# Kernel optimization log

Hardware: AMD Instinct MI355X
Metric: run time of the kernel (lower is better)

## Reference

```python
import jax, jax.numpy as jnp
import numpy as np

N, E, F_IN, F_E, H = 50000, 800000, 128, 16, 64
NEG_SLOPE = 0.2


def _glorot(key, shape):
    fan_in, fan_out = shape[0], shape[-1]
    lim = np.sqrt(6.0 / (fan_in + fan_out))
    return jax.random.uniform(key, shape, jnp.float32, -lim, lim)


def setup_inputs() -> dict:
    key = jax.random.key(0)
    ks = jax.random.split(key, 24)
    inp = {
        "x": jax.random.normal(ks[0], (N, F_IN), jnp.float32),
        "edge_index": jax.random.randint(ks[1], (2, E), 0, N, jnp.int64),
        "edge_attr": jax.random.normal(ks[2], (E, F_E), jnp.float32),
    }
    k = 3
    for i, f_in in zip((1, 2, 3), (F_IN, H, H)):
        inp[f"W{i}"] = _glorot(ks[k], (f_in, H)); k += 1
        inp[f"as{i}"] = _glorot(ks[k], (H,)); k += 1
        inp[f"ad{i}"] = _glorot(ks[k], (H,)); k += 1
        inp[f"We{i}"] = _glorot(ks[k], (F_E, H)); k += 1
        inp[f"ae{i}"] = _glorot(ks[k], (H,)); k += 1
        inp[f"b{i}"] = jnp.zeros((H,), jnp.float32)
        k += 1
    return inp


def gat_conv(x, src, dst, ea, W, a_s, a_d, We, a_e, b):
    # x: [N, f_in]; src/dst: [E'] (self-loops already appended); ea: [E', F_E]
    n = x.shape[0]
    h = x @ W                                   # [N, H]
    alpha_src = h @ a_s                          # [N]
    alpha_dst = h @ a_d                          # [N]
    alpha_e = (ea @ We) @ a_e                    # [E']
    alpha = alpha_src[src] + alpha_dst[dst] + alpha_e
    alpha = jnp.where(alpha > 0, alpha, NEG_SLOPE * alpha)  # leaky_relu
    # segment softmax over incoming edges of each dst node
    amax = jax.ops.segment_max(alpha, dst, num_segments=n)
    ex = jnp.exp(alpha - amax[dst])
    denom = jax.ops.segment_sum(ex, dst, num_segments=n)
    coef = ex / (denom[dst] + 1e-16)             # [E']
    out = jax.ops.segment_sum(h[src] * coef[:, None], dst, num_segments=n)
    return out + b


def reference(x, edge_index, edge_attr,
              W1, as1, ad1, We1, ae1, b1,
              W2, as2, ad2, We2, ae2, b2,
              W3, as3, ad3, We3, ae3, b3):
    n = x.shape[0]
    # add self-loops (PyG GATConv default), edge_attr fill_value='mean'
    loop = jnp.arange(n, dtype=edge_index.dtype)
    src = jnp.concatenate([edge_index[0], loop])
    dst = jnp.concatenate([edge_index[1], loop])
    ea_mean = jnp.mean(edge_attr, axis=0)
    ea = jnp.concatenate([edge_attr, jnp.broadcast_to(ea_mean, (n, edge_attr.shape[1]))], axis=0)

    x1 = jax.nn.elu(gat_conv(x, src, dst, ea, W1, as1, ad1, We1, ae1, b1))
    x2 = jax.nn.elu(gat_conv(x1, src, dst, ea, W2, as2, ad2, We2, ae2, b2))
    x3 = jax.nn.elu(gat_conv(x2, src, dst, ea, W3, as3, ad3, We3, ae3, b3))
    node_embeddings = x1 + x2 + x3
    graph_embedding = jnp.mean(node_embeddings, axis=0, keepdims=True)  # batch=None path
    return node_embeddings, graph_embedding
```

## Files before the change

### kernel.cpp

```cpp
#include <hip/hip_runtime.h>
#include <hip/hip_fp16.h>
#include <math.h>

#define HD 64
#define MAXNBK 512

typedef unsigned long long u64;
typedef _Float16 f16;
typedef _Float16 f16x8 __attribute__((ext_vector_type(8)));
typedef float f32x4 __attribute__((ext_vector_type(4)));

__device__ __forceinline__ u64 pack_rec(int src, float a0, float a1, float a2) {
    return (u64)(src & 0xFFFF)
         | ((u64)__half_as_ushort(__float2half(a0)) << 16)
         | ((u64)__half_as_ushort(__float2half(a1)) << 32)
         | ((u64)__half_as_ushort(__float2half(a2)) << 48);
}

__global__ void k_init(int* bcnt, float* gacc, int* tick, float* suG,
                       const float* We1, const float* ae1,
                       const float* We2, const float* ae2,
                       const float* We3, const float* ae3, int FE) {
    int t = threadIdx.x;
    for (int i = t; i < MAXNBK; i += 256) bcnt[i] = 0;
    if (t < HD) gacc[t] = 0.f;
    if (t == 0) *tick = 0;
    if (t < 3 * FE) {
        int l = t / FE, f = t % FE;
        const float* We = (l == 0) ? We1 : (l == 1) ? We2 : We3;
        const float* ae = (l == 0) ? ae1 : (l == 1) ? ae2 : ae3;
        float s = 0.f;
        for (int hh = 0; hh < HD; ++hh) s += We[f * HD + hh] * ae[hh];
        suG[t] = s;
    }
}

__global__ void k_pre(const int* __restrict__ ei, const float* __restrict__ ea,
                      const float* __restrict__ suG,
                      int E, int FE, u64* __restrict__ recE,
                      float* __restrict__ partials,
                      int ntiles, int chunk, int* bcnt, int NBK) {
    extern __shared__ float lds[];
    int t = threadIdx.x;

    if (blockIdx.x >= ntiles) {
        int* lc = (int*)lds;
        for (int i = t; i < NBK; i += 256) lc[i] = 0;
        __syncthreads();
        int cb = blockIdx.x - ntiles;
        int lo = cb * chunk, hi = min(E, lo + chunk);
        for (int e = lo + t; e < hi; e += 256)
            atomicAdd(&lc[ei[E + e] >> 7], 1);
        __syncthreads();
        for (int i = t; i < NBK; i += 256)
            if (lc[i]) atomicAdd(&bcnt[i], lc[i]);
        return;
    }

    float* sEA = lds;
    float* su = sEA + 256 * (FE + 1);
    float* colacc = su + 3 * FE;
    int ldE = FE + 1;

    if (t < 3 * FE) su[t] = suG[t];

    const float4* ea4 = (const float4*)ea;
    size_t tot4 = (size_t)E * FE / 4;
    int per_tile4 = 64 * FE;
    size_t base4 = (size_t)blockIdx.x * per_tile4;
    float4 acc = make_float4(0.f, 0.f, 0.f, 0.f);
    for (int i = t; i < per_tile4; i += 256) {
        size_t g4 = base4 + i;
        if (g4 < tot4) {
            float4 v = ea4[g4];
            acc.x += v.x; acc.y += v.y; acc.z += v.z; acc.w += v.w;
            int g = i * 4;
            int e_loc = g / FE, f = g % FE;
            float* p = &sEA[e_loc * ldE + f];
            p[0] = v.x; p[1] = v.y; p[2] = v.z; p[3] = v.w;
        }
    }
    colacc[t * 4 + 0] = acc.x; colacc[t * 4 + 1] = acc.y;
    colacc[t * 4 + 2] = acc.z; colacc[t * 4 + 3] = acc.w;
    __syncthreads();

    int e = blockIdx.x * 256 + t;
    if (e < E) {
        float a0 = 0.f, a1 = 0.f, a2 = 0.f;
        const float* row = &sEA[t * ldE];
        for (int f = 0; f < FE; ++f) {
            float v = row[f];
            a0 += v * su[f];
            a1 += v * su[FE + f];
            a2 += v * su[2 * FE + f];
        }
        int src = ei[e];
        recE[e] = pack_rec(src, a0, a1, a2);
    }
    if (t < 16) {
        int q = t >> 2, j = t & 3;
        float s = 0.f;
        for (int k = 0; k < 64; ++k) s += colacc[(q + k * 4) * 4 + j];
        partials[blockIdx.x * 16 + (q * 4 + j)] = s;
    }
}

__global__ void k_u2(const float* __restrict__ partials, int NB,
                     const float* __restrict__ suG,
                     float* sE, int FE, float invE,
                     const int* __restrict__ bcnt,
                     int* bfill , int* bbase, int NBK, int E) {
    __shared__ float red[256 * 4];
    __shared__ float mea[16];
    __shared__ int ib[256];
    int t = threadIdx.x;
    const float4* p4 = (const float4*)partials;
    int tot4 = NB * 4;
    float4 acc = make_float4(0.f, 0.f, 0.f, 0.f);
    for (int i = t; i < tot4; i += 256) {
        float4 v = p4[i];
        acc.x += v.x; acc.y += v.y; acc.z += v.z; acc.w += v.w;
    }
    red[t * 4 + 0] = acc.x; red[t * 4 + 1] = acc.y;
    red[t * 4 + 2] = acc.z; red[t * 4 + 3] = acc.w;
    int i0 = 2 * t, i1 = 2 * t + 1;
    int c0 = (i0 < NBK) ? bcnt[i0] : 0;
    int c1 = (i1 < NBK) ? bcnt[i1] : 0;
    ib[t] = c0 + c1;
    __syncthreads();
    for (int d = 1; d < 256; d <<= 1) {
        int x = (t >= d) ? ib[t - d] : 0;
        __syncthreads();
        ib[t] += x;
        __syncthreads();
    }
    int excl = ib[t] - (c0 + c1);
    if (i0 < NBK) { bbase[i0] = excl;      bfill[i0 * 16] = excl; }
    if (i1 < NBK) { bbase[i1] = excl + c0; bfill[i1 * 16] = excl + c0; }
    if (t == 0) bbase[NBK] = E;
    if (t < 16) {
        int q = t >> 2, j = t & 3;
        float s = 0.f;
        for (int k = 0; k < 64; ++k) s += red[(q + k * 4) * 4 + j];
        mea[q * 4 + j] = s * invE;
    }
    __syncthreads();
    if (t < 3) {
        float a = 0.f;
        for (int f = 0; f < FE; ++f) a += mea[f] * suG[t * FE + f];
        sE[t] = a;
    }
}

__global__ void k_bucket(const int* __restrict__ ei, const u64* __restrict__ recE,
                         int E, int chunk, int* bfill ,
                         u64* __restrict__ binned, unsigned char* __restrict__ bdstl,
                         int NBK) {
    __shared__ int lcnt[MAXNBK], gb[MAXNBK], lrank[MAXNBK];
    int t = threadIdx.x;
    for (int i = t; i < NBK; i += 256) lcnt[i] = 0;
    __syncthreads();
    int lo = blockIdx.x * chunk, hi = min(E, lo + chunk);
    for (int e = lo + t; e < hi; e += 256)
        atomicAdd(&lcnt[ei[E + e] >> 7], 1);
    __syncthreads();
    for (int i = t; i < NBK; i += 256) {
        lrank[i] = 0;
        gb[i] = lcnt[i] ? atomicAdd(&bfill[i * 16], lcnt[i]) : 0;
    }
    __syncthreads();
    for (int e = lo + t; e < hi; e += 256) {
        u64 r = recE[e];
        int dst = ei[E + e];
        int b = dst >> 7;
        int rank = atomicAdd(&lrank[b], 1);
        int pos = gb[b] + rank;
        binned[pos] = r;
        bdstl[pos] = (unsigned char)(dst & 127);
    }
}

__global__ void k_sort(const int* __restrict__ bbase, const u64* __restrict__ binned,
                       const unsigned char* __restrict__ bdstl,
                       const float* __restrict__ sE,
                       int* __restrict__ row_ptr,
                       u64* __restrict__ rec, int N, int E) {
    __shared__ int lcnt[128], lfill[128];
    int b = blockIdx.x, t = threadIdx.x;
    int base = bbase[b], nrec = bbase[b + 1] - base;
    if (t < 128) lcnt[t] = 0;
    __syncthreads();
    for (int i = t; i < nrec; i += 256)
        atomicAdd(&lcnt[bdstl[base + i]], 1);
    __syncthreads();
    int v = (t < 128) ? lcnt[t] : 0;
    for (int d = 1; d < 128; d <<= 1) {
        int x = (t >= d && t < 128) ? lcnt[t - d] : 0;
        __syncthreads();
        if (t < 128) lcnt[t] += x;
        __syncthreads();
    }
    int gnode = (b << 7) + t;
    if (t < 128) {
        int rp = base + gnode + (lcnt[t] - v);
        if (gnode < N) {
            row_ptr[gnode] = rp;
            rec[rp] = pack_rec(gnode, sE[0], sE[1], sE[2]);
        }
        lfill[t] = rp + 1;
    }
    if (b == 0 && t == 0) row_ptr[N] = E + N;
    __syncthreads();
    for (int i = t; i < nrec; i += 256) {
        u64 r = binned[base + i];
        int dl = bdstl[base + i];
        int p = atomicAdd(&lfill[dl], 1);
        rec[p] = r;
    }
}

__global__ void k_gemm(const void* __restrict__ xin, int in_f16,
                       const float* __restrict__ W,
                       const float* __restrict__ a_s, const float* __restrict__ a_d,
                       __half* __restrict__ h, float* __restrict__ as_n,
                       float* __restrict__ ad_n, int N, int K) {
    extern __shared__ char smem[];
    const int SK = K + 8;
    f16* xs = (f16*)smem;
    f16* wt = xs + 64 * SK;
    int t = threadIdx.x;
    int nb = blockIdx.x * 64;

    int nK4 = K >> 2;
    if (in_f16) {
        const __half* xh = (const __half*)xin;
        for (int i = t; i < 64 * nK4; i += 256) {
            int row = i / nK4, c4 = i % nK4;
            int gr = nb + row; if (gr >= N) gr = N - 1;
            u64 v = ((const u64*)(xh + (size_t)gr * K))[c4];
            *(u64*)&xs[row * SK + c4 * 4] = v;
        }
    } else {
        const float* xf = (const float*)xin;
        for (int i = t; i < 64 * nK4; i += 256) {
            int row = i / nK4, c4 = i % nK4;
            int gr = nb + row; if (gr >= N) gr = N - 1;
            float4 v = ((const float4*)(xf + (size_t)gr * K))[c4];
            f16* p = &xs[row * SK + c4 * 4];
            p[0] = (f16)v.x; p[1] = (f16)v.y; p[2] = (f16)v.z; p[3] = (f16)v.w;
        }
    }
    for (int i = t; i < K * 64; i += 256) {
        int k = i >> 6, c = i & 63;
        wt[c * SK + k] = (f16)W[i];
    }
    __syncthreads();

    int wv = t >> 6, lane = t & 63;
    int m = lane & 15, quad = lane >> 4;
    int rowA = wv * 16 + m;

    f32x4 acc[4];
#pragma unroll
    for (int ct = 0; ct < 4; ++ct) acc[ct] = (f32x4){0.f, 0.f, 0.f, 0.f};

    for (int ks = 0; ks < (K >> 5); ++ks) {
        f16x8 a = *(const f16x8*)&xs[rowA * SK + ks * 32 + quad * 8];
#pragma unroll
        for (int ct = 0; ct < 4; ++ct) {
            f16x8 bf = *(const f16x8*)&wt[(ct * 16 + m) * SK + ks * 32 + quad * 8];
            acc[ct] = __builtin_amdgcn_mfma_f32_16x16x32_f16(a, bf, acc[ct], 0, 0, 0);
        }
    }

    {
        float as_c[4], ad_c[4];
#pragma unroll
        for (int ct = 0; ct < 4; ++ct) {
            as_c[ct] = a_s[ct * 16 + m];
            ad_c[ct] = a_d[ct * 16 + m];
        }
#pragma unroll
        for (int r = 0; r < 4; ++r) {
            float ps = acc[0][r] * as_c[0] + acc[1][r] * as_c[1]
                     + acc[2][r] * as_c[2] + acc[3][r] * as_c[3];
            float pd = acc[0][r] * ad_c[0] + acc[1][r] * ad_c[1]
                     + acc[2][r] * ad_c[2] + acc[3][r] * ad_c[3];
#pragma unroll
            for (int dd = 8; dd; dd >>= 1) {
                ps += __shfl_xor(ps, dd, 64);
                pd += __shfl_xor(pd, dd, 64);
            }
            if (m == 0) {
                int gr = nb + wv * 16 + quad * 4 + r;
                if (gr < N) { as_n[gr] = ps; ad_n[gr] = pd; }
            }
        }
    }

    __syncthreads();
    f16* ht = xs;
    const int HS = 72;
#pragma unroll
    for (int ct = 0; ct < 4; ++ct)
#pragma unroll
        for (int r = 0; r < 4; ++r) {
            int rl = wv * 16 + quad * 4 + r;
            ht[rl * HS + ct * 16 + m] = (f16)acc[ct][r];
        }
    __syncthreads();

    {
        int row = t >> 2, cb = (t & 3) * 16;
        int gr = nb + row;
        if (gr < N) {
            ulonglong2 v0 = *(const ulonglong2*)&ht[row * HS + cb];
            ulonglong2 v1 = *(const ulonglong2*)&ht[row * HS + cb + 8];
            *(ulonglong2*)(h + (size_t)gr * HD + cb) = v0;
            *(ulonglong2*)(h + (size_t)gr * HD + cb + 8) = v1;
        }
    }
}

__global__ void k_aggr(const __half* __restrict__ h, const float* __restrict__ as_n,
                       const float* __restrict__ ad_n, const int* __restrict__ row_ptr,
                       const u64* __restrict__ rec, int l,
                       const float* __restrict__ b, __half* __restrict__ x_out,
                       float* __restrict__ emb, int N, int first) {
    int wave = threadIdx.x >> 6, lane = threadIdx.x & 63;
    int n = blockIdx.x * 4 + wave;
    if (n >= N) return;
    int base = row_ptr[n], end = row_ptr[n + 1];
    float adv = ad_n[n];
    const int shift = 16 * (l + 1);
    int qq = lane >> 4, fq = lane & 15;
    float m = -INFINITY, d = 0.f;
    f32x4 acc = {0.f, 0.f, 0.f, 0.f};

    for (int c = base; c < end; c += 64) {
        int cnt = min(64, end - c);
        float a = -INFINITY;
        int s = 0;
        if (lane < cnt) {
            u64 r = rec[c + lane];
            s = (int)(r & 0xFFFFull);
            float aE = __half2float(__ushort_as_half((unsigned short)(r >> shift)));
            a = as_n[s] + adv + aE;
            a = (a > 0.f) ? a : 0.2f * a;
        }
        float mc = a;
#pragma unroll
        for (int dd = 32; dd; dd >>= 1) mc = fmaxf(mc, __shfl_xor(mc, dd, 64));
        float mn = fmaxf(m, mc);
        float w = (lane < cnt) ? __expf(a - mn) : 0.f;
        float dc = w;
#pragma unroll
        for (int dd = 32; dd; dd >>= 1) dc += __shfl_xor(dc, dd, 64);
        float sc = __expf(m - mn);
        d = d * sc + dc;
        acc[0] *= sc; acc[1] *= sc; acc[2] *= sc; acc[3] *= sc;
        m = mn;
        int iters = (cnt + 3) >> 2;
        for (int j4 = 0; j4 < iters; ++j4) {
            int j = (j4 << 2) + qq;
            int sj = __shfl(s, j, 64);
            float wj = __shfl(w, j, 64);
            u64 hv = *(const u64*)(h + (size_t)sj * HD + (fq << 2));
            __half2 h0 = *(__half2*)&hv;
            __half2 h1 = *((__half2*)&hv + 1);
            float2 f0 = __half22float2(h0);
            float2 f1 = __half22float2(h1);
            acc[0] += wj * f0.x; acc[1] += wj * f0.y;
            acc[2] += wj * f1.x; acc[3] += wj * f1.y;
        }
    }

#pragma unroll
    for (int cc = 0; cc < 4; ++cc) {
        acc[cc] += __shfl_xor(acc[cc], 32, 64);
        acc[cc] += __shfl_xor(acc[cc], 16, 64);
    }
    float inv = 1.f / (d + 1e-16f);
    float4 b4 = ((const float4*)b)[fq];
    float v0 = acc[0] * inv + b4.x; v0 = (v0 > 0.f) ? v0 : expm1f(v0);
    float v1 = acc[1] * inv + b4.y; v1 = (v1 > 0.f) ? v1 : expm1f(v1);
    float v2 = acc[2] * inv + b4.z; v2 = (v2 > 0.f) ? v2 : expm1f(v2);
    float v3 = acc[3] * inv + b4.w; v3 = (v3 > 0.f) ? v3 : expm1f(v3);
    if (qq == 0) {
        union { u64 u; __half2 h2[2]; } ou;
        ou.h2[0] = __floats2half2_rn(v0, v1);
        ou.h2[1] = __floats2half2_rn(v2, v3);
        *(u64*)(x_out + (size_t)n * HD + (fq << 2)) = ou.u;
        float4* ep = (float4*)(emb + (size_t)n * HD) + fq;
        if (first) {
            *ep = make_float4(v0, v1, v2, v3);
        } else {
            float4 e = *ep;
            e.x += v0; e.y += v1; e.z += v2; e.w += v3;
            *ep = e;
        }
    }
}

__global__ void k_red(float* __restrict__ emb, float* __restrict__ gacc,
                      int* __restrict__ tick, int N) {
    __shared__ float lds[256];
    __shared__ int lastf;
    int f = threadIdx.x & 63, w = threadIdx.x >> 6;
    float s = 0.f;
    for (int n = blockIdx.x * 4 + w; n < N; n += gridDim.x * 4)
        s += emb[(size_t)n * HD + f];
    lds[threadIdx.x] = s;
    __syncthreads();
    if (w == 0) {
        float v = lds[f] + lds[64 + f] + lds[128 + f] + lds[192 + f];
        atomicAdd(&gacc[f], v);
    }
    __syncthreads();
    __threadfence();
    if (threadIdx.x == 0)
        lastf = (atomicAdd(tick, 1) == (int)gridDim.x - 1);
    __syncthreads();
    if (lastf && threadIdx.x < HD) {
        float g = __hip_atomic_load(&gacc[threadIdx.x], __ATOMIC_RELAXED,
                                    __HIP_MEMORY_SCOPE_AGENT);
        emb[(size_t)N * HD + threadIdx.x] = g / (float)N;
    }
}

extern "C" void kernel_launch(void* const* d_in, const int* in_sizes, int n_in,
                              void* d_out, int out_size, void* d_ws, size_t ws_size,
                              hipStream_t stream) {
    const float* x = (const float*)d_in[0];
    const int* ei = (const int*)d_in[1];
    const float* ea = (const float*)d_in[2];

    const int FIN = in_sizes[3] / HD;
    const int N = in_sizes[0] / FIN;
    const int E = in_sizes[1] / 2;
    const int FE = in_sizes[2] / E;
    const int NBK = (N + 127) >> 7;
    const int NPRE = 512;

    const float* W[3];  const float* as_[3]; const float* ad_[3];
    const float* We[3]; const float* ae_[3]; const float* bb[3];
    for (int l = 0; l < 3; ++l) {
        W[l]  = (const float*)d_in[3 + 6 * l + 0];
        as_[l] = (const float*)d_in[3 + 6 * l + 1];
        ad_[l] = (const float*)d_in[3 + 6 * l + 2];
        We[l] = (const float*)d_in[3 + 6 * l + 3];
        ae_[l] = (const float*)d_in[3 + 6 * l + 4];
        bb[l] = (const float*)d_in[3 + 6 * l + 5];
    }

    int ntiles = (E + 255) / 256;
    int chunk = (E + NPRE - 1) / NPRE;

    char* ws = (char*)d_ws;
    size_t off = 0;
    auto alloc = [&](size_t bytes) {
        void* p = ws + off;
        off += (bytes + 255) & ~(size_t)255;
        return p;
    };
    __half* h      = (__half*)alloc((size_t)N * HD * 2);
    __half* x_cur  = (__half*)alloc((size_t)N * HD * 2);
    float*  as_n   = (float*)alloc((size_t)N * 4);
    float*  ad_n   = (float*)alloc((size_t)N * 4);
    int*    rowp   = (int*)alloc((size_t)(N + 1) * 4);
    int*    bcnt   = (int*)alloc((size_t)MAXNBK * 4);
    int*    bfill  = (int*)alloc((size_t)MAXNBK * 16 * 4);
    int*    bbase  = (int*)alloc((size_t)(MAXNBK + 1) * 4);
    u64*    rec    = (u64*)alloc((size_t)(E + N) * 8);
    u64*    recE   = (u64*)alloc((size_t)E * 8);
    u64*    binned = (u64*)alloc((size_t)E * 8);
    unsigned char* bdstl = (unsigned char*)alloc((size_t)E);
    float*  partials = (float*)alloc((size_t)ntiles * 16 * 4);
    float*  sE     = (float*)alloc(3 * 4);
    float*  gacc   = (float*)alloc(HD * 4);
    float*  suG    = (float*)alloc(3 * 16 * 4);
    int*    tick   = (int*)alloc(4);
    (void)ws_size; (void)n_in; (void)out_size;

    float* emb = (float*)d_out;

    k_init<<<1, 256, 0, stream>>>(bcnt, gacc, tick, suG,
                                  We[0], ae_[0], We[1], ae_[1], We[2], ae_[2], FE);
    size_t pre_lds = (size_t)(256 * (FE + 1) + 3 * FE + 256 * 4) * 4;
    k_pre<<<ntiles + NPRE, 256, pre_lds, stream>>>(ei, ea, suG, E, FE, recE, partials,
                                                   ntiles, chunk, bcnt, NBK);
    k_u2<<<1, 256, 0, stream>>>(partials, ntiles, suG, sE, FE, 1.0f / (float)E,
                                bcnt, bfill, bbase, NBK, E);
    k_bucket<<<NPRE, 256, 0, stream>>>(ei, recE, E, chunk, bfill, binned, bdstl, NBK);
    k_sort<<<NBK, 256, 0, stream>>>(bbase, binned, bdstl, sE, rowp, rec, N, E);

    for (int l = 0; l < 3; ++l) {
        const void* xin = (l == 0) ? (const void*)x : (const void*)x_cur;
        int in_f16 = (l == 0) ? 0 : 1;
        int K = (l == 0) ? FIN : HD;
        size_t ldsz = (size_t)(2 * 64 * (K + 8)) * 2;
        k_gemm<<<(N + 63) / 64, 256, ldsz, stream>>>(xin, in_f16, W[l], as_[l], ad_[l],
                                                     h, as_n, ad_n, N, K);
        k_aggr<<<(N + 3) / 4, 256, 0, stream>>>(h, as_n, ad_n, rowp, rec, l,
                                                bb[l], x_cur, emb, N, (l == 0) ? 1 : 0);
    }

    k_red<<<256, 256, 0, stream>>>(emb, gacc, tick, N);
}
```

Before: 378.6 us.

## Fuse layer-1 GEMM into preprocessing kernel and widen aggregation loads

Layer 1's projection GEMM now runs as extra blocks inside the edge preprocessing launch. This removes one kernel launch and lets the GEMM overlap with the edge-attribute and bucket-count work. The aggregation kernel now has each lane load 8 halves (16 bytes) per neighbour and processes 8 neighbours per wave step instead of 4, which widens memory transactions. The LDS allocation for the fused kernel is sized to the larger of the two uses, which may reduce occupancy.

```diff
diff --git a/kernel.cpp b/kernel.cpp
--- a/kernel.cpp
+++ b/kernel.cpp
@@ -35,19 +35,111 @@
     }
 }
 
-__global__ void k_pre(const int* __restrict__ ei, const float* __restrict__ ea,
-                      const float* __restrict__ suG,
-                      int E, int FE, u64* __restrict__ recE,
-                      float* __restrict__ partials,
-                      int ntiles, int chunk, int* bcnt, int NBK) {
-    extern __shared__ float lds[];
+__global__ void k_preX(const int* __restrict__ ei, const float* __restrict__ ea,
+                       const float* __restrict__ suG,
+                       int E, int FE, u64* __restrict__ recE,
+                       float* __restrict__ partials,
+                       int ntiles, int chunk, int* bcnt, int NBK,
+                       int Gg, const float* __restrict__ x,
+                       const float* __restrict__ W,
+                       const float* __restrict__ a_s, const float* __restrict__ a_d,
+                       __half* __restrict__ h, float* __restrict__ as_n,
+                       float* __restrict__ ad_n, int N, int K) {
+    extern __shared__ char smemraw[];
     int t = threadIdx.x;
 
-    if (blockIdx.x >= ntiles) {
-        int* lc = (int*)lds;
+    if (blockIdx.x < Gg) {
+        const int SK = K + 8;
+        f16* xs = (f16*)smemraw;
+        f16* wt = xs + 64 * SK;
+        int nb = blockIdx.x * 64;
+
+        int nK4 = K >> 2;
+        for (int i = t; i < 64 * nK4; i += 256) {
+            int row = i / nK4, c4 = i % nK4;
+            int gr = nb + row; if (gr >= N) gr = N - 1;
+            float4 v = ((const float4*)(x + (size_t)gr * K))[c4];
+            f16* p = &xs[row * SK + c4 * 4];
+            p[0] = (f16)v.x; p[1] = (f16)v.y; p[2] = (f16)v.z; p[3] = (f16)v.w;
+        }
+        for (int i = t; i < K * 64; i += 256) {
+            int k = i >> 6, c = i & 63;
+            wt[c * SK + k] = (f16)W[i];
+        }
+        __syncthreads();
+
+        int wv = t >> 6, lane = t & 63;
+        int m = lane & 15, quad = lane >> 4;
+        int rowA = wv * 16 + m;
+
+        f32x4 acc[4];
+#pragma unroll
+        for (int ct = 0; ct < 4; ++ct) acc[ct] = (f32x4){0.f, 0.f, 0.f, 0.f};
+
+        for (int ks = 0; ks < (K >> 5); ++ks) {
+            f16x8 a = *(const f16x8*)&xs[rowA * SK + ks * 32 + quad * 8];
+#pragma unroll
+            for (int ct = 0; ct < 4; ++ct) {
+                f16x8 bf = *(const f16x8*)&wt[(ct * 16 + m) * SK + ks * 32 + quad * 8];
+                acc[ct] = __builtin_amdgcn_mfma_f32_16x16x32_f16(a, bf, acc[ct], 0, 0, 0);
+            }
+        }
+
+        {
+            float as_c[4], ad_c[4];
+#pragma unroll
+            for (int ct = 0; ct < 4; ++ct) {
+                as_c[ct] = a_s[ct * 16 + m];
+                ad_c[ct] = a_d[ct * 16 + m];
+            }
+#pragma unroll
+            for (int r = 0; r < 4; ++r) {
+                float ps = acc[0][r] * as_c[0] + acc[1][r] * as_c[1]
+                         + acc[2][r] * as_c[2] + acc[3][r] * as_c[3];
+                float pd = acc[0][r] * ad_c[0] + acc[1][r] * ad_c[1]
+                         + acc[2][r] * ad_c[2] + acc[3][r] * ad_c[3];
+#pragma unroll
+                for (int dd = 8; dd; dd >>= 1) {
+                    ps += __shfl_xor(ps, dd, 64);
+                    pd += __shfl_xor(pd, dd, 64);
+                }
+                if (m == 0) {
+                    int gr = nb + wv * 16 + quad * 4 + r;
+                    if (gr < N) { as_n[gr] = ps; ad_n[gr] = pd; }
+                }
+            }
+        }
+
+        __syncthreads();
+        f16* ht = xs;
+        const int HS = 72;
+#pragma unroll
+        for (int ct = 0; ct < 4; ++ct)
+#pragma unroll
+            for (int r = 0; r < 4; ++r) {
+                int rl = wv * 16 + quad * 4 + r;
+                ht[rl * HS + ct * 16 + m] = (f16)acc[ct][r];
+            }
+        __syncthreads();
+        {
+            int row = t >> 2, cb = (t & 3) * 16;
+            int gr = nb + row;
+            if (gr < N) {
+                ulonglong2 v0 = *(const ulonglong2*)&ht[row * HS + cb];
+                ulonglong2 v1 = *(const ulonglong2*)&ht[row * HS + cb + 8];
+                *(ulonglong2*)(h + (size_t)gr * HD + cb) = v0;
+                *(ulonglong2*)(h + (size_t)gr * HD + cb + 8) = v1;
+            }
+        }
+        return;
+    }
+
+    int bx = blockIdx.x - Gg;
+    if (bx >= ntiles) {
+        int* lc = (int*)smemraw;
         for (int i = t; i < NBK; i += 256) lc[i] = 0;
         __syncthreads();
-        int cb = blockIdx.x - ntiles;
+        int cb = bx - ntiles;
         int lo = cb * chunk, hi = min(E, lo + chunk);
         for (int e = lo + t; e < hi; e += 256)
             atomicAdd(&lc[ei[E + e] >> 7], 1);
@@ -57,6 +149,7 @@
         return;
     }
 
+    float* lds = (float*)smemraw;
     float* sEA = lds;
     float* su = sEA + 256 * (FE + 1);
     float* colacc = su + 3 * FE;
@@ -67,7 +160,7 @@
     const float4* ea4 = (const float4*)ea;
     size_t tot4 = (size_t)E * FE / 4;
     int per_tile4 = 64 * FE;
-    size_t base4 = (size_t)blockIdx.x * per_tile4;
+    size_t base4 = (size_t)bx * per_tile4;
     float4 acc = make_float4(0.f, 0.f, 0.f, 0.f);
     for (int i = t; i < per_tile4; i += 256) {
         size_t g4 = base4 + i;
@@ -84,7 +177,7 @@
     colacc[t * 4 + 2] = acc.z; colacc[t * 4 + 3] = acc.w;
     __syncthreads();
 
-    int e = blockIdx.x * 256 + t;
+    int e = bx * 256 + t;
     if (e < E) {
         float a0 = 0.f, a1 = 0.f, a2 = 0.f;
         const float* row = &sEA[t * ldE];
@@ -101,7 +194,7 @@
         int q = t >> 2, j = t & 3;
         float s = 0.f;
         for (int k = 0; k < 64; ++k) s += colacc[(q + k * 4) * 4 + j];
-        partials[blockIdx.x * 16 + (q * 4 + j)] = s;
+        partials[bx * 16 + (q * 4 + j)] = s;
     }
 }
 
@@ -219,7 +312,7 @@
     }
 }
 
-__global__ void k_gemm(const void* __restrict__ xin, int in_f16,
+__global__ void k_gemm(const __half* __restrict__ xin,
                        const float* __restrict__ W,
                        const float* __restrict__ a_s, const float* __restrict__ a_d,
                        __half* __restrict__ h, float* __restrict__ as_n,
@@ -232,23 +325,11 @@
     int nb = blockIdx.x * 64;
 
     int nK4 = K >> 2;
-    if (in_f16) {
-        const __half* xh = (const __half*)xin;
-        for (int i = t; i < 64 * nK4; i += 256) {
-            int row = i / nK4, c4 = i % nK4;
-            int gr = nb + row; if (gr >= N) gr = N - 1;
-            u64 v = ((const u64*)(xh + (size_t)gr * K))[c4];
-            *(u64*)&xs[row * SK + c4 * 4] = v;
-        }
-    } else {
-        const float* xf = (const float*)xin;
-        for (int i = t; i < 64 * nK4; i += 256) {
-            int row = i / nK4, c4 = i % nK4;
-            int gr = nb + row; if (gr >= N) gr = N - 1;
-            float4 v = ((const float4*)(xf + (size_t)gr * K))[c4];
-            f16* p = &xs[row * SK + c4 * 4];
-            p[0] = (f16)v.x; p[1] = (f16)v.y; p[2] = (f16)v.z; p[3] = (f16)v.w;
-        }
+    for (int i = t; i < 64 * nK4; i += 256) {
+        int row = i / nK4, c4 = i % nK4;
+        int gr = nb + row; if (gr >= N) gr = N - 1;
+        u64 v = ((const u64*)(xin + (size_t)gr * K))[c4];
+        *(u64*)&xs[row * SK + c4 * 4] = v;
     }
     for (int i = t; i < K * 64; i += 256) {
         int k = i >> 6, c = i & 63;
@@ -333,9 +414,11 @@
     int base = row_ptr[n], end = row_ptr[n + 1];
     float adv = ad_n[n];
     const int shift = 16 * (l + 1);
-    int qq = lane >> 4, fq = lane & 15;
+    int qq = lane >> 3, fo = lane & 7;
     float m = -INFINITY, d = 0.f;
-    f32x4 acc = {0.f, 0.f, 0.f, 0.f};
+    float acc[8];
+#pragma unroll
+    for (int k = 0; k < 8; ++k) acc[k] = 0.f;
 
     for (int c = base; c < end; c += 64) {
         int cnt = min(64, end - c);
@@ -358,46 +441,55 @@
         for (int dd = 32; dd; dd >>= 1) dc += __shfl_xor(dc, dd, 64);
         float sc = __expf(m - mn);
         d = d * sc + dc;
-        acc[0] *= sc; acc[1] *= sc; acc[2] *= sc; acc[3] *= sc;
+#pragma unroll
+        for (int k = 0; k < 8; ++k) acc[k] *= sc;
         m = mn;
-        int iters = (cnt + 3) >> 2;
-        for (int j4 = 0; j4 < iters; ++j4) {
-            int j = (j4 << 2) + qq;
+        int iters = (cnt + 7) >> 3;
+        for (int j8 = 0; j8 < iters; ++j8) {
+            int j = (j8 << 3) + qq;
             int sj = __shfl(s, j, 64);
             float wj = __shfl(w, j, 64);
-            u64 hv = *(const u64*)(h + (size_t)sj * HD + (fq << 2));
-            __half2 h0 = *(__half2*)&hv;
-            __half2 h1 = *((__half2*)&hv + 1);
-            float2 f0 = __half22float2(h0);
-            float2 f1 = __half22float2(h1);
-            acc[0] += wj * f0.x; acc[1] += wj * f0.y;
-            acc[2] += wj * f1.x; acc[3] += wj * f1.y;
-        }
-    }
-
-#pragma unroll
-    for (int cc = 0; cc < 4; ++cc) {
-        acc[cc] += __shfl_xor(acc[cc], 32, 64);
-        acc[cc] += __shfl_xor(acc[cc], 16, 64);
-    }
-    float inv = 1.f / (d + 1e-16f);
-    float4 b4 = ((const float4*)b)[fq];
-    float v0 = acc[0] * inv + b4.x; v0 = (v0 > 0.f) ? v0 : expm1f(v0);
-    float v1 = acc[1] * inv + b4.y; v1 = (v1 > 0.f) ? v1 : expm1f(v1);
-    float v2 = acc[2] * inv + b4.z; v2 = (v2 > 0.f) ? v2 : expm1f(v2);
-    float v3 = acc[3] * inv + b4.w; v3 = (v3 > 0.f) ? v3 : expm1f(v3);
+            ulonglong2 hv = *(const ulonglong2*)(h + (size_t)sj * HD + (fo << 3));
+            __half2* hp = (__half2*)&hv;
+#pragma unroll
+            for (int k = 0; k < 4; ++k) {
+                float2 f = __half22float2(hp[k]);
+                acc[2 * k]     += wj * f.x;
+                acc[2 * k + 1] += wj * f.y;
+            }
+        }
+    }
+
+#pragma unroll
+    for (int k = 0; k < 8; ++k) {
+        acc[k] += __shfl_xor(acc[k], 8, 64);
+        acc[k] += __shfl_xor(acc[k], 16, 64);
+        acc[k] += __shfl_xor(acc[k], 32, 64);
+    }
     if (qq == 0) {
-        union { u64 u; __half2 h2[2]; } ou;
-        ou.h2[0] = __floats2half2_rn(v0, v1);
-        ou.h2[1] = __floats2half2_rn(v2, v3);
-        *(u64*)(x_out + (size_t)n * HD + (fq << 2)) = ou.u;
-        float4* ep = (float4*)(emb + (size_t)n * HD) + fq;
+        float inv = 1.f / (d + 1e-16f);
+        const float4* b4p = (const float4*)(b + (fo << 3));
+        float4 b0 = b4p[0], b1 = b4p[1];
+        float bb[8] = {b0.x, b0.y, b0.z, b0.w, b1.x, b1.y, b1.z, b1.w};
+        float vv[8];
+#pragma unroll
+        for (int k = 0; k < 8; ++k) {
+            float v = acc[k] * inv + bb[k];
+            vv[k] = (v > 0.f) ? v : expm1f(v);
+        }
+        union { unsigned short us[8]; ulonglong2 u2; } ou;
+#pragma unroll
+        for (int k = 0; k < 8; ++k) ou.us[k] = __half_as_ushort(__float2half(vv[k]));
+        *(ulonglong2*)(x_out + (size_t)n * HD + (fo << 3)) = ou.u2;
+        float4* ep = (float4*)(emb + (size_t)n * HD + (fo << 3));
         if (first) {
-            *ep = make_float4(v0, v1, v2, v3);
+            ep[0] = make_float4(vv[0], vv[1], vv[2], vv[3]);
+            ep[1] = make_float4(vv[4], vv[5], vv[6], vv[7]);
         } else {
-            float4 e = *ep;
-            e.x += v0; e.y += v1; e.z += v2; e.w += v3;
-            *ep = e;
+            float4 e0 = ep[0], e1 = ep[1];
+            e0.x += vv[0]; e0.y += vv[1]; e0.z += vv[2]; e0.w += vv[3];
+            e1.x += vv[4]; e1.y += vv[5]; e1.z += vv[6]; e1.w += vv[7];
+            ep[0] = e0; ep[1] = e1;
         }
     }
 }
@@ -455,6 +547,7 @@
 
     int ntiles = (E + 255) / 256;
     int chunk = (E + NPRE - 1) / NPRE;
+    int Gg = (N + 63) / 64;
 
     char* ws = (char*)d_ws;
     size_t off = 0;
@@ -487,20 +580,22 @@
     k_init<<<1, 256, 0, stream>>>(bcnt, gacc, tick, suG,
                                   We[0], ae_[0], We[1], ae_[1], We[2], ae_[2], FE);
     size_t pre_lds = (size_t)(256 * (FE + 1) + 3 * FE + 256 * 4) * 4;
-    k_pre<<<ntiles + NPRE, 256, pre_lds, stream>>>(ei, ea, suG, E, FE, recE, partials,
-                                                   ntiles, chunk, bcnt, NBK);
+    size_t g0_lds = (size_t)(2 * 64 * (FIN + 8)) * 2;
+    size_t fused_lds = pre_lds > g0_lds ? pre_lds : g0_lds;
+    k_preX<<<Gg + ntiles + NPRE, 256, fused_lds, stream>>>(
+        ei, ea, suG, E, FE, recE, partials, ntiles, chunk, bcnt, NBK,
+        Gg, x, W[0], as_[0], ad_[0], h, as_n, ad_n, N, FIN);
     k_u2<<<1, 256, 0, stream>>>(partials, ntiles, suG, sE, FE, 1.0f / (float)E,
                                 bcnt, bfill, bbase, NBK, E);
     k_bucket<<<NPRE, 256, 0, stream>>>(ei, recE, E, chunk, bfill, binned, bdstl, NBK);
     k_sort<<<NBK, 256, 0, stream>>>(bbase, binned, bdstl, sE, rowp, rec, N, E);
 
     for (int l = 0; l < 3; ++l) {
-        const void* xin = (l == 0) ? (const void*)x : (const void*)x_cur;
-        int in_f16 = (l == 0) ? 0 : 1;
-        int K = (l == 0) ? FIN : HD;
-        size_t ldsz = (size_t)(2 * 64 * (K + 8)) * 2;
-        k_gemm<<<(N + 63) / 64, 256, ldsz, stream>>>(xin, in_f16, W[l], as_[l], ad_[l],
-                                                     h, as_n, ad_n, N, K);
+        if (l > 0) {
+            size_t ldsz = (size_t)(2 * 64 * (HD + 8)) * 2;
+            k_gemm<<<(N + 63) / 64, 256, ldsz, stream>>>(x_cur, W[l], as_[l], ad_[l],
+                                                         h, as_n, ad_n, N, HD);
+        }
         k_aggr<<<(N + 3) / 4, 256, 0, stream>>>(h, as_n, ad_n, rowp, rec, l,
                                                 bb[l], x_cur, emb, N, (l == 0) ? 1 : 0);
     }
```

Measured after the change: 383.5 us. About the same (+1.3%).

## Store node features as fp32 and aggregate with packed FMA over 8 edges per step

Applied to the files above, without the earlier changes.

The GEMM now writes h directly in fp32 from MFMA accumulators, with no LDS staging and no fp16 conversion. The aggregation kernel reads 8 floats per lane, handles 8 edges per iteration instead of 4, and accumulates with v_pk_fma_f32 inline asm. The aim is to drop the half-to-float conversions and LDS round-trips and to halve the gather loop count. In exchange, the gathered feature table doubles in size and the GEMM writes become strided scalar stores.

```diff
diff --git a/kernel.cpp b/kernel.cpp
--- a/kernel.cpp
+++ b/kernel.cpp
@@ -9,6 +9,7 @@
 typedef _Float16 f16;
 typedef _Float16 f16x8 __attribute__((ext_vector_type(8)));
 typedef float f32x4 __attribute__((ext_vector_type(4)));
+typedef float f32x2 __attribute__((ext_vector_type(2)));
 
 __device__ __forceinline__ u64 pack_rec(int src, float a0, float a1, float a2) {
     return (u64)(src & 0xFFFF)
@@ -222,7 +223,7 @@
 __global__ void k_gemm(const void* __restrict__ xin, int in_f16,
                        const float* __restrict__ W,
                        const float* __restrict__ a_s, const float* __restrict__ a_d,
-                       __half* __restrict__ h, float* __restrict__ as_n,
+                       float* __restrict__ h32, float* __restrict__ as_n,
                        float* __restrict__ ad_n, int N, int K) {
     extern __shared__ char smem[];
     const int SK = K + 8;
@@ -298,31 +299,16 @@
         }
     }
 
-    __syncthreads();
-    f16* ht = xs;
-    const int HS = 72;
 #pragma unroll
     for (int ct = 0; ct < 4; ++ct)
 #pragma unroll
         for (int r = 0; r < 4; ++r) {
-            int rl = wv * 16 + quad * 4 + r;
-            ht[rl * HS + ct * 16 + m] = (f16)acc[ct][r];
-        }
-    __syncthreads();
-
-    {
-        int row = t >> 2, cb = (t & 3) * 16;
-        int gr = nb + row;
-        if (gr < N) {
-            ulonglong2 v0 = *(const ulonglong2*)&ht[row * HS + cb];
-            ulonglong2 v1 = *(const ulonglong2*)&ht[row * HS + cb + 8];
-            *(ulonglong2*)(h + (size_t)gr * HD + cb) = v0;
-            *(ulonglong2*)(h + (size_t)gr * HD + cb + 8) = v1;
-        }
-    }
-}
-
-__global__ void k_aggr(const __half* __restrict__ h, const float* __restrict__ as_n,
+            int gr = nb + wv * 16 + quad * 4 + r;
+            if (gr < N) h32[(size_t)gr * HD + ct * 16 + m] = acc[ct][r];
+        }
+}
+
+__global__ void k_aggr(const float* __restrict__ h32, const float* __restrict__ as_n,
                        const float* __restrict__ ad_n, const int* __restrict__ row_ptr,
                        const u64* __restrict__ rec, int l,
                        const float* __restrict__ b, __half* __restrict__ x_out,
@@ -333,9 +319,11 @@
     int base = row_ptr[n], end = row_ptr[n + 1];
     float adv = ad_n[n];
     const int shift = 16 * (l + 1);
-    int qq = lane >> 4, fq = lane & 15;
+    int qq = lane >> 3, fo = lane & 7;
     float m = -INFINITY, d = 0.f;
-    f32x4 acc = {0.f, 0.f, 0.f, 0.f};
+    f32x2 acc2[4];
+#pragma unroll
+    for (int k = 0; k < 4; ++k) acc2[k] = (f32x2){0.f, 0.f};
 
     for (int c = base; c < end; c += 64) {
         int cnt = min(64, end - c);
@@ -358,46 +346,58 @@
         for (int dd = 32; dd; dd >>= 1) dc += __shfl_xor(dc, dd, 64);
         float sc = __expf(m - mn);
         d = d * sc + dc;
-        acc[0] *= sc; acc[1] *= sc; acc[2] *= sc; acc[3] *= sc;
+#pragma unroll
+        for (int k = 0; k < 4; ++k) acc2[k] = acc2[k] * sc;
         m = mn;
-        int iters = (cnt + 3) >> 2;
-        for (int j4 = 0; j4 < iters; ++j4) {
-            int j = (j4 << 2) + qq;
+        int iters = (cnt + 7) >> 3;
+        for (int j8 = 0; j8 < iters; ++j8) {
+            int j = (j8 << 3) + qq;
             int sj = __shfl(s, j, 64);
             float wj = __shfl(w, j, 64);
-            u64 hv = *(const u64*)(h + (size_t)sj * HD + (fq << 2));
-            __half2 h0 = *(__half2*)&hv;
-            __half2 h1 = *((__half2*)&hv + 1);
-            float2 f0 = __half22float2(h0);
-            float2 f1 = __half22float2(h1);
-            acc[0] += wj * f0.x; acc[1] += wj * f0.y;
-            acc[2] += wj * f1.x; acc[3] += wj * f1.y;
-        }
-    }
-
-#pragma unroll
-    for (int cc = 0; cc < 4; ++cc) {
-        acc[cc] += __shfl_xor(acc[cc], 32, 64);
-        acc[cc] += __shfl_xor(acc[cc], 16, 64);
-    }
-    float inv = 1.f / (d + 1e-16f);
-    float4 b4 = ((const float4*)b)[fq];
-    float v0 = acc[0] * inv + b4.x; v0 = (v0 > 0.f) ? v0 : expm1f(v0);
-    float v1 = acc[1] * inv + b4.y; v1 = (v1 > 0.f) ? v1 : expm1f(v1);
-    float v2 = acc[2] * inv + b4.z; v2 = (v2 > 0.f) ? v2 : expm1f(v2);
-    float v3 = acc[3] * inv + b4.w; v3 = (v3 > 0.f) ? v3 : expm1f(v3);
+            f32x2 w2; w2.x = wj; w2.y = wj;
+            const float* hrow = h32 + (size_t)sj * HD + (fo << 3);
+            f32x2 hv[4];
+            *(f32x4*)&hv[0] = *(const f32x4*)hrow;
+            *(f32x4*)&hv[2] = *(const f32x4*)(hrow + 4);
+#pragma unroll
+            for (int k = 0; k < 4; ++k)
+                asm("v_pk_fma_f32 %0, %1, %2, %0"
+                    : "+v"(acc2[k]) : "v"(w2), "v"(hv[k]));
+        }
+    }
+
+#pragma unroll
+    for (int k = 0; k < 4; ++k) {
+#pragma unroll
+        for (int dd = 8; dd <= 32; dd <<= 1) {
+            acc2[k].x += __shfl_xor(acc2[k].x, dd, 64);
+            acc2[k].y += __shfl_xor(acc2[k].y, dd, 64);
+        }
+    }
     if (qq == 0) {
-        union { u64 u; __half2 h2[2]; } ou;
-        ou.h2[0] = __floats2half2_rn(v0, v1);
-        ou.h2[1] = __floats2half2_rn(v2, v3);
-        *(u64*)(x_out + (size_t)n * HD + (fq << 2)) = ou.u;
-        float4* ep = (float4*)(emb + (size_t)n * HD) + fq;
+        float inv = 1.f / (d + 1e-16f);
+        const float4* b4p = (const float4*)(b + (fo << 3));
+        float4 b0 = b4p[0], b1 = b4p[1];
+        float bb[8] = {b0.x, b0.y, b0.z, b0.w, b1.x, b1.y, b1.z, b1.w};
+        float vv[8];
+#pragma unroll
+        for (int k = 0; k < 8; ++k) {
+            float v = ((k & 1) ? acc2[k >> 1].y : acc2[k >> 1].x) * inv + bb[k];
+            vv[k] = (v > 0.f) ? v : expm1f(v);
+        }
+        union { unsigned short us[8]; ulonglong2 u2; } ou;
+#pragma unroll
+        for (int k = 0; k < 8; ++k) ou.us[k] = __half_as_ushort(__float2half(vv[k]));
+        *(ulonglong2*)(x_out + (size_t)n * HD + (fo << 3)) = ou.u2;
+        float4* ep = (float4*)(emb + (size_t)n * HD + (fo << 3));
         if (first) {
-            *ep = make_float4(v0, v1, v2, v3);
+            ep[0] = make_float4(vv[0], vv[1], vv[2], vv[3]);
+            ep[1] = make_float4(vv[4], vv[5], vv[6], vv[7]);
         } else {
-            float4 e = *ep;
-            e.x += v0; e.y += v1; e.z += v2; e.w += v3;
-            *ep = e;
+            float4 e0 = ep[0], e1 = ep[1];
+            e0.x += vv[0]; e0.y += vv[1]; e0.z += vv[2]; e0.w += vv[3];
+            e1.x += vv[4]; e1.y += vv[5]; e1.z += vv[6]; e1.w += vv[7];
+            ep[0] = e0; ep[1] = e1;
         }
     }
 }
@@ -463,7 +463,7 @@
         off += (bytes + 255) & ~(size_t)255;
         return p;
     };
-    __half* h      = (__half*)alloc((size_t)N * HD * 2);
+    float*  h32    = (float*)alloc((size_t)N * HD * 4);
     __half* x_cur  = (__half*)alloc((size_t)N * HD * 2);
     float*  as_n   = (float*)alloc((size_t)N * 4);
     float*  ad_n   = (float*)alloc((size_t)N * 4);
@@ -500,8 +500,8 @@
         int K = (l == 0) ? FIN : HD;
         size_t ldsz = (size_t)(2 * 64 * (K + 8)) * 2;
         k_gemm<<<(N + 63) / 64, 256, ldsz, stream>>>(xin, in_f16, W[l], as_[l], ad_[l],
-                                                     h, as_n, ad_n, N, K);
-        k_aggr<<<(N + 3) / 4, 256, 0, stream>>>(h, as_n, ad_n, rowp, rec, l,
+                                                     h32, as_n, ad_n, N, K);
+        k_aggr<<<(N + 3) / 4, 256, 0, stream>>>(h32, as_n, ad_n, rowp, rec, l,
                                                 bb[l], x_cur, emb, N, (l == 0) ? 1 : 0);
     }
 
```

After: 402.9 us. 1.06x slower.
